# Optimization experiments

Hardware: AMD Instinct MI355X
Metric: run time of the kernel (lower is better)

## Reference

```python
import jax, jax.numpy as jnp
import numpy as np

B, S, D = 4, 2048, 1024
H, HD = 16, 64
NDIM = 2                      # 2D RoPE (position_ids last dim)
PER_DIM = 2 * (HD // (2 * NDIM))   # 32 rotated dims per spatial axis
HALF = PER_DIM // 2                # 16
EPS = 1e-6


def setup_inputs() -> dict:
    key = jax.random.key(0)
    ks = jax.random.split(key, 10)
    sc = 0.02
    return {
        "hidden_states": jax.random.normal(ks[0], (B, S, D), jnp.float32),
        "cos": jax.random.uniform(ks[1], (B, S, HD), jnp.float32, -1.0, 1.0),
        "sin": jax.random.uniform(ks[2], (B, S, HD), jnp.float32, -1.0, 1.0),
        "position_ids": jax.random.randint(ks[3], (B, S, NDIM), 0, S, jnp.int64 if jax.config.x64_enabled else jnp.int32),
        # torch nn.Linear weights are [out_features, in_features]
        "wq": jax.random.normal(ks[4], (H * HD, D), jnp.float32) * sc,
        "wk": jax.random.normal(ks[5], (H * HD, D), jnp.float32) * sc,
        "wv": jax.random.normal(ks[6], (H * HD, D), jnp.float32) * sc,
        "wo": jax.random.normal(ks[7], (D, H * HD), jnp.float32) * sc,
        "q_scale": jnp.ones((HD,), jnp.float32),
        "k_scale": jnp.ones((HD,), jnp.float32),
    }


def _rms_norm(x, scale=None, eps=EPS):
    n = x * jax.lax.rsqrt(jnp.mean(x * x, axis=-1, keepdims=True) + eps)
    return n * scale if scale is not None else n


def _rotate_half(x):
    x1, x2 = x[..., :HALF], x[..., HALF:]
    return jnp.concatenate([-x2, x1], axis=-1)


def _rope2d(x, cos, sin):
    # x: [B,S,H,HD]; cos/sin: [B,S,HD]; rotate each NDIM chunk independently
    parts = []
    for k in range(NDIM):
        sl = slice(k * PER_DIM, (k + 1) * PER_DIM)
        xp = x[..., sl]
        cp = cos[:, :, None, sl]
        sp = sin[:, :, None, sl]
        parts.append(xp * cp + _rotate_half(xp) * sp)
    return jnp.concatenate(parts, axis=-1)


def reference(hidden_states, cos, sin, position_ids, wq, wk, wv, wo, q_scale, k_scale):
    b, s, _ = hidden_states.shape
    # QKV projections (clamp buffers default to +/-inf -> identity)
    q = (hidden_states @ wq.T).reshape(b, s, H, HD)
    k = (hidden_states @ wk.T).reshape(b, s, H, HD)
    v = (hidden_states @ wv.T).reshape(b, s, H, HD)
    # per-head RMSNorm (q/k with scale, v without)
    q = _rms_norm(q, q_scale)
    k = _rms_norm(k, k_scale)
    v = _rms_norm(v)
    # 2D RoPE on q and k
    q = _rope2d(q, cos, sin)
    k = _rope2d(k, cos, sin)
    # SDPA with scale=1.0 (as in the source), heads-major layout
    scores = jnp.einsum('bqhd,bkhd->bhqk', q, k)
    attn = jax.nn.softmax(scores, axis=-1)
    out = jnp.einsum('bhqk,bkhd->bqhd', attn, v).reshape(b, s, H * HD)
    return out @ wo.T
```

## Files before the change

### kernel.cpp

```cpp
#include <hip/hip_runtime.h>
#include <hip/hip_bf16.h>
#include <stdint.h>
#include <stddef.h>

#define B_ 4
#define S_ 2048
#define D_ 1024
#define H_ 16
#define HD_ 64
#define NTOK (B_*S_)
#define HDIM (H_*HD_)
#define LOG2E 1.44269504088896f

typedef __bf16 bf16_t;
typedef __bf16 bf16x4 __attribute__((ext_vector_type(4)));
typedef __bf16 bf16x8 __attribute__((ext_vector_type(8)));
typedef float floatx4 __attribute__((ext_vector_type(4)));

#define MFMA16(a,b,c)  __builtin_amdgcn_mfma_f32_16x16x32_bf16((a),(b),(c),0,0,0)

__device__ __forceinline__ void async_cp16(const bf16_t* g, bf16_t* l) {
    typedef __attribute__((address_space(1))) const unsigned int gu32;
    typedef __attribute__((address_space(3))) unsigned int lu32;
    __builtin_amdgcn_global_load_lds((gu32*)g, (lu32*)l, 16, 0, 0);
}

__device__ __forceinline__ bf16x8 cat44(bf16x4 a, bf16x4 b) {
    union { bf16x4 h[2]; bf16x8 v; } u;
    u.h[0] = a; u.h[1] = b;
    return u.v;
}

struct Cvt6 {
    const float* s[5]; bf16_t* d[5]; int n4[5];
    const float* cs; const float* sn; float* cpk;
};

__global__ __launch_bounds__(256) void cvt6(Cvt6 p) {
    const int z = blockIdx.y;
    if (z < 5) {
        const float4* __restrict__ src = (const float4*)p.s[z];
        bf16x4* __restrict__ dst = (bf16x4*)p.d[z];
        const int n4 = p.n4[z];
        for (int i = blockIdx.x * 256 + threadIdx.x; i < n4; i += gridDim.x * 256) {
            const float4 v = src[i];
            dst[i] = (bf16x4){(bf16_t)v.x, (bf16_t)v.y, (bf16_t)v.z, (bf16_t)v.w};
        }
    } else {
        const int N = B_*S_*HD_;
        for (int i = blockIdx.x * 256 + threadIdx.x; i < N; i += gridDim.x * 256) {
            const int bs = i >> 6, d = i & 63;
            float2 cs2;
            cs2.x = p.cs[i];
            cs2.y = p.sn[i];
            *(float2*)(p.cpk + (size_t)bs*128 + (d & 15)*8 + (d >> 4)*2) = cs2;
        }
    }
}

struct GemmPtrs {
    const bf16_t* A[3]; const bf16_t* W[3]; void* C[3];
    const float* cpk; const float* qs; const float* ks;
};

template<int MODE>
__global__ __launch_bounds__(256, 3) void gemm_nt(GemmPtrs p, int K) {
    __shared__ bf16_t lds[4*4096];
    bf16_t* lA0 = lds;
    bf16_t* lA1 = lds + 4096;
    bf16_t* lB0 = lds + 8192;
    bf16_t* lB1 = lds + 12288;
    const bf16_t* __restrict__ A = p.A[blockIdx.z];
    const bf16_t* __restrict__ W = p.W[blockIdx.z];
    const int m0 = blockIdx.y * 128;
    const int n0 = blockIdx.x * 128;
    const int t = threadIdx.x;
    const int lane = t & 63;
    const int wave = t >> 6;
    const int wm = wave >> 1;
    const int wn = wave & 1;
    const int l16 = lane & 15;
    const int quad = lane >> 4;

    const int srow0 = wave*32 + (lane >> 2);
    const int skc   = (lane & 3) * 8;

    floatx4 acc[4][4] = {};

    for (int k0 = 0; k0 < K; k0 += 64) {
        #pragma unroll
        for (int c = 0; c < 2; ++c) {
            const int row = srow0 + c*16;
            const size_t ao = (size_t)(m0+row)*K + k0 + skc;
            const size_t wo = (size_t)(n0+row)*K + k0 + skc;
            async_cp16(&A[ao],      &lA0[row*32 + skc]);
            async_cp16(&A[ao + 32], &lA1[row*32 + skc]);
            async_cp16(&W[wo],      &lB0[row*32 + skc]);
            async_cp16(&W[wo + 32], &lB1[row*32 + skc]);
        }
        __syncthreads();
        {
            bf16x8 af[4], bfr[4];
            #pragma unroll
            for (int i = 0; i < 4; ++i) {
                af[i]  = *(const bf16x8*)(&lA0[(wm*64 + i*16 + l16)*32 + quad*8]);
                bfr[i] = *(const bf16x8*)(&lB0[(wn*64 + i*16 + l16)*32 + quad*8]);
            }
            #pragma unroll
            for (int i = 0; i < 4; ++i)
                #pragma unroll
                for (int j = 0; j < 4; ++j)
                    acc[i][j] = MFMA16(af[i], bfr[j], acc[i][j]);
        }
        {
            bf16x8 af[4], bfr[4];
            #pragma unroll
            for (int i = 0; i < 4; ++i) {
                af[i]  = *(const bf16x8*)(&lA1[(wm*64 + i*16 + l16)*32 + quad*8]);
                bfr[i] = *(const bf16x8*)(&lB1[(wn*64 + i*16 + l16)*32 + quad*8]);
            }
            #pragma unroll
            for (int i = 0; i < 4; ++i)
                #pragma unroll
                for (int j = 0; j < 4; ++j)
                    acc[i][j] = MFMA16(af[i], bfr[j], acc[i][j]);
        }
        __syncthreads();
    }

    if (MODE == 1) {
        const int z = blockIdx.z;
        const int h = blockIdx.x*2 + wn;
        float inv[4][4];
        #pragma unroll
        for (int i = 0; i < 4; ++i) {
            #pragma unroll
            for (int r = 0; r < 4; ++r) {
                float ssq = 0.f;
                #pragma unroll
                for (int j = 0; j < 4; ++j) ssq += acc[i][j][r]*acc[i][j][r];
                ssq += __shfl_xor(ssq, 1);
                ssq += __shfl_xor(ssq, 2);
                ssq += __shfl_xor(ssq, 4);
                ssq += __shfl_xor(ssq, 8);
                inv[i][r] = rsqrtf(ssq*(1.f/64.f) + 1e-6f);
            }
        }
        if (z < 2) {
            bf16_t* __restrict__ C = (bf16_t*)p.C[z];
            const float* __restrict__ scp = (z == 0) ? p.qs : p.ks;
            const float scl = (z == 0) ? LOG2E : 1.f;
            float qsl[4];
            #pragma unroll
            for (int j = 0; j < 4; ++j) qsl[j] = scp[j*16 + l16] * scl;
            #pragma unroll
            for (int i = 0; i < 4; ++i) {
                #pragma unroll
                for (int r = 0; r < 4; ++r) {
                    const int m = m0 + wm*64 + i*16 + quad*4 + r;
                    const int b = m >> 11, s = m & (S_-1);
                    float nv[4];
                    #pragma unroll
                    for (int j = 0; j < 4; ++j) nv[j] = acc[i][j][r] * inv[i][r] * qsl[j];
                    const float* cb = p.cpk + ((size_t)b*S_ + s)*128 + l16*8;
                    const float4 L0 = *(const float4*)(cb);
                    const float4 L1 = *(const float4*)(cb + 4);
                    bf16_t* crow = &C[(((size_t)b*H_ + h)*S_ + s)*HD_ + l16];
                    crow[0]  = (bf16_t)(nv[0]*L0.x - nv[1]*L0.y);
                    crow[16] = (bf16_t)(nv[1]*L0.z + nv[0]*L0.w);
                    crow[32] = (bf16_t)(nv[2]*L1.x - nv[3]*L1.y);
                    crow[48] = (bf16_t)(nv[3]*L1.z + nv[2]*L1.w);
                }
            }
        } else {
            bf16_t* __restrict__ Vt = (bf16_t*)p.C[2];
            const int mbase = m0 + wm*64;
            const int b = mbase >> 11;
            const int sbase = mbase & (S_-1);
            bf16_t* wl = lds + wave*2304;
            #pragma unroll
            for (int ps = 0; ps < 2; ++ps) {
                #pragma unroll
                for (int jj = 0; jj < 2; ++jj) {
                    const int j = ps*2 + jj;
                    const int dd = jj*16 + l16;
                    #pragma unroll
                    for (int i = 0; i < 4; ++i) {
                        bf16x4 pk;
                        #pragma unroll
                        for (int r = 0; r < 4; ++r)
                            pk[r] = (bf16_t)(acc[i][j][r] * inv[i][r]);
                        *(bf16x4*)(&wl[dd*72 + i*16 + quad*4]) = pk;
                    }
                }
                const int dloc = lane >> 1;
                const int kh = (lane & 1) * 32;
                bf16_t* dst = &Vt[((size_t)(b*H_ + h)*HD_ + ps*32 + dloc)*S_ + sbase + kh];
                #pragma unroll
                for (int c = 0; c < 4; ++c) {
                    const bf16x8 vv = *(const bf16x8*)(&wl[dloc*72 + kh + c*8]);
                    *(bf16x8*)(&dst[c*8]) = vv;
                }
            }
        }
    } else {
        float* __restrict__ C = (float*)p.C[blockIdx.z];
        #pragma unroll
        for (int i = 0; i < 4; ++i) {
            const int mb = m0 + wm*64 + i*16 + quad*4;
            #pragma unroll
            for (int j = 0; j < 4; ++j) {
                const int n = n0 + wn*64 + j*16 + l16;
                #pragma unroll
                for (int r = 0; r < 4; ++r)
                    C[(size_t)(mb + r)*HDIM + n] = acc[i][j][r];
            }
        }
    }
}

__global__ __launch_bounds__(512, 4) void flash_attn(
    const bf16_t* __restrict__ qn, const bf16_t* __restrict__ kn,
    const bf16_t* __restrict__ vt, bf16_t* __restrict__ attn_out) {
    __shared__ __align__(16) bf16_t sh[16384];

    const int bh = blockIdx.y;
    const int b  = bh >> 4;
    const int h  = bh & 15;
    const int q0 = blockIdx.x * 256;
    const int t = threadIdx.x;
    const int wave = t >> 6;
    const int lane = t & 63;
    const int l16 = lane & 15;
    const int quad = lane >> 4;
    const floatx4 finit = {-46.f, -46.f, -46.f, -46.f};

    const bf16_t* Q  = qn + (size_t)bh * S_ * HD_;
    const bf16_t* K  = kn + (size_t)bh * S_ * HD_;
    const bf16_t* Vt = vt + (size_t)bh * HD_ * S_;

    bf16x8 qf[2][2];
    #pragma unroll
    for (int rb = 0; rb < 2; ++rb) {
        const int qrow = q0 + wave*32 + rb*16 + l16;
        qf[rb][0] = *(const bf16x8*)(&Q[(size_t)qrow*HD_ + quad*8]);
        qf[rb][1] = *(const bf16x8*)(&Q[(size_t)qrow*HD_ + 32 + quad*8]);
    }

    floatx4 accO[2][4] = {};
    float accL[2] = {0.f, 0.f};

    const int sgrow = (wave & 3)*16 + l16;
    const int sgcol = (wave >> 2)*32 + quad*8;
    const int kwoff = (wave & 3)*1024 + (wave >> 2)*512 + lane*8;
    const int vU    = ((wave & 3)*2 + (wave >> 2))*64 + ((2*quad) & 3)*16 + l16;
    const int vwoff = vU*8 + (quad >> 1)*4;

    async_cp16(&K[(size_t)sgrow*HD_ + sgcol], &sh[kwoff]);
    {
        const bf16x8 v0 = *(const bf16x8*)(&Vt[(size_t)sgrow*S_ + sgcol]);
        union { bf16x8 v; bf16x4 hh[2]; } uv; uv.v = v0;
        *(bf16x4*)(&sh[8192 + vwoff])       = uv.hh[0];
        *(bf16x4*)(&sh[8192 + vwoff + 128]) = uv.hh[1];
    }

    bf16x8 vpre;
    for (int i = 0; i < S_/64; ++i) {
        __syncthreads();
        const bf16_t* lK = sh + (i & 1)*4096;
        const bf16_t* lV = sh + 8192 + (i & 1)*4096;
        const bool more = (i + 1 < S_/64);
        if (more) {
            const int ktn = (i + 1) * 64;
            async_cp16(&K[(size_t)(ktn + sgrow)*HD_ + sgcol],
                       &sh[((i+1) & 1)*4096 + kwoff]);
            vpre = *(const bf16x8*)(&Vt[(size_t)sgrow*S_ + ktn + sgcol]);
        }

        __builtin_amdgcn_s_setprio(1);
        bf16x4 pf[2][4];
        #pragma unroll
        for (int ct = 0; ct < 4; ++ct) {
            const bf16x8 kf0 = *(const bf16x8*)(&lK[ct*1024 + lane*8]);
            const bf16x8 kf1 = *(const bf16x8*)(&lK[ct*1024 + 512 + lane*8]);
            #pragma unroll
            for (int rb = 0; rb < 2; ++rb) {
                floatx4 s = MFMA16(kf0, qf[rb][0], finit);
                s = MFMA16(kf1, qf[rb][1], s);
                const float e0 = __builtin_amdgcn_exp2f(s[0]);
                const float e1 = __builtin_amdgcn_exp2f(s[1]);
                const float e2 = __builtin_amdgcn_exp2f(s[2]);
                const float e3 = __builtin_amdgcn_exp2f(s[3]);
                accL[rb] += (e0 + e1) + (e2 + e3);
                bf16x4 pb;
                pb[0] = (bf16_t)e0; pb[1] = (bf16_t)e1;
                pb[2] = (bf16_t)e2; pb[3] = (bf16_t)e3;
                pf[rb][ct] = pb;
            }
        }
        bf16x8 pb8[2][2];
        #pragma unroll
        for (int rb = 0; rb < 2; ++rb) {
            pb8[rb][0] = cat44(pf[rb][0], pf[rb][1]);
            pb8[rb][1] = cat44(pf[rb][2], pf[rb][3]);
        }
        #pragma unroll
        for (int dt = 0; dt < 4; ++dt) {
            #pragma unroll
            for (int c = 0; c < 2; ++c) {
                const bf16x8 vf = *(const bf16x8*)(&lV[(dt*2 + c)*512 + lane*8]);
                accO[0][dt] = MFMA16(vf, pb8[0][c], accO[0][dt]);
                accO[1][dt] = MFMA16(vf, pb8[1][c], accO[1][dt]);
            }
        }
        __builtin_amdgcn_s_setprio(0);

        if (more) {
            bf16_t* nV = sh + 8192 + ((i+1) & 1)*4096;
            union { bf16x8 v; bf16x4 hh[2]; } uv; uv.v = vpre;
            *(bf16x4*)(&nV[vwoff])       = uv.hh[0];
            *(bf16x4*)(&nV[vwoff + 128]) = uv.hh[1];
        }
    }

    __syncthreads();
    bf16_t* W = sh + wave * (16*72);
    #pragma unroll
    for (int rb = 0; rb < 2; ++rb) {
        float lr = accL[rb];
        lr += __shfl_xor(lr, 16);
        lr += __shfl_xor(lr, 32);
        const float inv = 1.f / lr;
        #pragma unroll
        for (int dt = 0; dt < 4; ++dt)
            #pragma unroll
            for (int r = 0; r < 4; ++r)
                W[l16*72 + dt*16 + quad*4 + r] = (bf16_t)(accO[rb][dt][r] * inv);
        #pragma unroll
        for (int half = 0; half < 2; ++half) {
            const int qr = half*8 + (lane >> 3);
            const bf16x8 o = *(const bf16x8*)(&W[qr*72 + (lane & 7)*8]);
            const int srw = q0 + wave*32 + rb*16 + qr;
            *(bf16x8*)(&attn_out[((size_t)b*S_ + srw)*HDIM + h*HD_ + (lane & 7)*8]) = o;
        }
    }
}

extern "C" void kernel_launch(void* const* d_in, const int* in_sizes, int n_in,
                              void* d_out, int out_size, void* d_ws, size_t ws_size,
                              hipStream_t stream) {
    (void)in_sizes; (void)n_in; (void)out_size; (void)ws_size;
    const float* X  = (const float*)d_in[0];
    const float* cs = (const float*)d_in[1];
    const float* sn = (const float*)d_in[2];
    const float* wq = (const float*)d_in[4];
    const float* wk = (const float*)d_in[5];
    const float* wv = (const float*)d_in[6];
    const float* wo = (const float*)d_in[7];
    const float* qs = (const float*)d_in[8];
    const float* ks = (const float*)d_in[9];
    float* out = (float*)d_out;

    const size_t PROJ = (size_t)NTOK * HDIM;
    const size_t WSZ  = (size_t)HDIM * D_;
    bf16_t* ws   = (bf16_t*)d_ws;
    bf16_t* Xb   = ws;
    bf16_t* wqb  = ws + PROJ;
    bf16_t* wkb  = wqb + WSZ;
    bf16_t* wvb  = wkb + WSZ;
    bf16_t* wob  = wvb + WSZ;
    bf16_t* qb   = wob + WSZ;
    bf16_t* kb   = qb + PROJ;
    bf16_t* vb   = kb + PROJ;
    bf16_t* vt   = vb;
    bf16_t* attn = Xb;
    float*  cpk  = out;

    Cvt6 cp;
    cp.s[0] = X;  cp.d[0] = Xb;  cp.n4[0] = (int)(PROJ/4);
    cp.s[1] = wq; cp.d[1] = wqb; cp.n4[1] = (int)(WSZ/4);
    cp.s[2] = wk; cp.d[2] = wkb; cp.n4[2] = (int)(WSZ/4);
    cp.s[3] = wv; cp.d[3] = wvb; cp.n4[3] = (int)(WSZ/4);
    cp.s[4] = wo; cp.d[4] = wob; cp.n4[4] = (int)(WSZ/4);
    cp.cs = cs; cp.sn = sn; cp.cpk = cpk;
    cvt6<<<dim3(1024, 6), 256, 0, stream>>>(cp);

    GemmPtrs g1;
    g1.A[0] = Xb;  g1.A[1] = Xb;  g1.A[2] = Xb;
    g1.W[0] = wqb; g1.W[1] = wkb; g1.W[2] = wvb;
    g1.C[0] = qb;  g1.C[1] = kb;  g1.C[2] = vt;
    g1.cpk = cpk; g1.qs = qs; g1.ks = ks;
    gemm_nt<1><<<dim3(HDIM/128, NTOK/128, 3), 256, 0, stream>>>(g1, D_);

    flash_attn<<<dim3(S_/256, B_*H_), 512, 0, stream>>>(qb, kb, vt, attn);

    GemmPtrs g2;
    g2.A[0] = attn; g2.W[0] = wob; g2.C[0] = out;
    g2.A[1] = attn; g2.W[1] = wob; g2.C[1] = out;
    g2.A[2] = attn; g2.W[2] = wob; g2.C[2] = out;
    g2.cpk = cpk; g2.qs = qs; g2.ks = ks;
    gemm_nt<2><<<dim3(HDIM/128, NTOK/128, 1), 256, 0, stream>>>(g2, HDIM);
}
```

Measured before the change: 285.2 us.

## Swizzle GEMM LDS layout and remap block indices for XCD-aware scheduling

The GEMM gathers K-chunks from global memory with an XOR swizzle on the column offset so that LDS fragment reads use a matching XOR. This is meant to reduce LDS bank conflicts while keeping the async global-to-LDS copy destinations contiguous. Both the GEMM and flash attention kernels now remap the linear block index so that consecutive blocks, which are spread across XCDs round-robin, share row blocks or (batch, head) pairs and so reuse L2. The remapping hardcodes an 8x8 tile grid and 64 bh, so it assumes the fixed problem shape.

```diff
diff --git a/kernel.cpp b/kernel.cpp
--- a/kernel.cpp
+++ b/kernel.cpp
@@ -72,8 +72,12 @@
     bf16_t* lB1 = lds + 12288;
     const bf16_t* __restrict__ A = p.A[blockIdx.z];
     const bf16_t* __restrict__ W = p.W[blockIdx.z];
-    const int m0 = blockIdx.y * 128;
-    const int n0 = blockIdx.x * 128;
+    const int lin  = blockIdx.x + 8*blockIdx.y;
+    const int slot = lin >> 3;
+    const int mblk = (lin & 7)*8 + (slot >> 3);
+    const int nblk = slot & 7;
+    const int m0 = mblk * 128;
+    const int n0 = nblk * 128;
     const int t = threadIdx.x;
     const int lane = t & 63;
     const int wave = t >> 6;
@@ -84,6 +88,8 @@
 
     const int srow0 = wave*32 + (lane >> 2);
     const int skc   = (lane & 3) * 8;
+    const int gsw   = ((srow0 ^ (srow0 >> 2)) & 3) * 8;
+    const int glw   = ((l16 ^ (l16 >> 2)) & 3) * 8;
 
     floatx4 acc[4][4] = {};
 
@@ -91,8 +97,8 @@
         #pragma unroll
         for (int c = 0; c < 2; ++c) {
             const int row = srow0 + c*16;
-            const size_t ao = (size_t)(m0+row)*K + k0 + skc;
-            const size_t wo = (size_t)(n0+row)*K + k0 + skc;
+            const size_t ao = (size_t)(m0+row)*K + k0 + (skc ^ gsw);
+            const size_t wo = (size_t)(n0+row)*K + k0 + (skc ^ gsw);
             async_cp16(&A[ao],      &lA0[row*32 + skc]);
             async_cp16(&A[ao + 32], &lA1[row*32 + skc]);
             async_cp16(&W[wo],      &lB0[row*32 + skc]);
@@ -103,8 +109,8 @@
             bf16x8 af[4], bfr[4];
             #pragma unroll
             for (int i = 0; i < 4; ++i) {
-                af[i]  = *(const bf16x8*)(&lA0[(wm*64 + i*16 + l16)*32 + quad*8]);
-                bfr[i] = *(const bf16x8*)(&lB0[(wn*64 + i*16 + l16)*32 + quad*8]);
+                af[i]  = *(const bf16x8*)(&lA0[(wm*64 + i*16 + l16)*32 + (quad*8 ^ glw)]);
+                bfr[i] = *(const bf16x8*)(&lB0[(wn*64 + i*16 + l16)*32 + (quad*8 ^ glw)]);
             }
             #pragma unroll
             for (int i = 0; i < 4; ++i)
@@ -116,8 +122,8 @@
             bf16x8 af[4], bfr[4];
             #pragma unroll
             for (int i = 0; i < 4; ++i) {
-                af[i]  = *(const bf16x8*)(&lA1[(wm*64 + i*16 + l16)*32 + quad*8]);
-                bfr[i] = *(const bf16x8*)(&lB1[(wn*64 + i*16 + l16)*32 + quad*8]);
+                af[i]  = *(const bf16x8*)(&lA1[(wm*64 + i*16 + l16)*32 + (quad*8 ^ glw)]);
+                bfr[i] = *(const bf16x8*)(&lB1[(wn*64 + i*16 + l16)*32 + (quad*8 ^ glw)]);
             }
             #pragma unroll
             for (int i = 0; i < 4; ++i)
@@ -130,7 +136,7 @@
 
     if (MODE == 1) {
         const int z = blockIdx.z;
-        const int h = blockIdx.x*2 + wn;
+        const int h = nblk*2 + wn;
         float inv[4][4];
         #pragma unroll
         for (int i = 0; i < 4; ++i) {
@@ -224,10 +230,12 @@
     const bf16_t* __restrict__ vt, bf16_t* __restrict__ attn_out) {
     __shared__ __align__(16) bf16_t sh[16384];
 
-    const int bh = blockIdx.y;
+    const int lin  = blockIdx.x + 8*blockIdx.y;
+    const int slot = lin >> 3;
+    const int bh   = (lin & 7)*8 + (slot >> 3);
+    const int q0   = (slot & 7) * 256;
     const int b  = bh >> 4;
     const int h  = bh & 15;
-    const int q0 = blockIdx.x * 256;
     const int t = threadIdx.x;
     const int wave = t >> 6;
     const int lane = t & 63;
```

Result: faster. 258.2 us (-9.5%).
